# Performance work log

Hardware: AMD Instinct MI355X
Metric: run time of the kernel (lower is better)

The kernel has to match this reference:

```python
import jax, jax.numpy as jnp
import numpy as np

HIDDEN = 1280
NUM_HEADS = 16
NUM_KV_HEADS = 4
HEAD_DIM = 80
Q_SIZE = NUM_HEADS * HEAD_DIM          # 1280
KV_SIZE = NUM_KV_HEADS * HEAD_DIM      # 320
QKV_OUT = Q_SIZE + 2 * KV_SIZE         # 1920
R_SOFTPLUS_0 = 1.442695041


def setup_inputs() -> dict:
    key = jax.random.key(0)
    ks = jax.random.split(key, 6)
    B, S = 4, 2048
    return {
        "hidden_states": jax.random.normal(ks[0], (B, S, HIDDEN), dtype=jnp.float32),
        "scaling": jax.random.normal(ks[1], (HEAD_DIM,), dtype=jnp.float32),
        "qkv_w": jax.random.normal(ks[2], (QKV_OUT, HIDDEN), dtype=jnp.float32) * (1.0 / np.sqrt(HIDDEN)),
        "qkv_b": jax.random.normal(ks[3], (QKV_OUT,), dtype=jnp.float32) * 0.01,
        "o_w": jax.random.normal(ks[4], (HIDDEN, Q_SIZE), dtype=jnp.float32) * (1.0 / np.sqrt(Q_SIZE)),
        "o_b": jax.random.normal(ks[5], (HIDDEN,), dtype=jnp.float32) * 0.01,
    }


def reference(hidden_states, scaling, qkv_w, qkv_b, o_w, o_b):
    B, S, _ = hidden_states.shape
    qkv = hidden_states @ qkv_w.T + qkv_b                      # [B,S,1920]
    xq = qkv[..., :Q_SIZE].reshape(B, S, NUM_HEADS, HEAD_DIM)
    xk = qkv[..., Q_SIZE:Q_SIZE + KV_SIZE].reshape(B, S, NUM_KV_HEADS, HEAD_DIM)
    xv = qkv[..., Q_SIZE + KV_SIZE:].reshape(B, S, NUM_KV_HEADS, HEAD_DIM)
    # learned per-head-dim scaling: (r_softplus_0/sqrt(d)) * softplus(scaling)
    scale = (R_SOFTPLUS_0 / np.sqrt(HEAD_DIM)) * jax.nn.softplus(scaling)
    xq = xq * scale[None, None, None, :]
    # GQA: expand kv heads to match query heads (repeat_interleave on head dim)
    nq_per_kv = NUM_HEADS // NUM_KV_HEADS
    k = jnp.repeat(xk, nq_per_kv, axis=2)                      # [B,S,H,d]
    v = jnp.repeat(xv, nq_per_kv, axis=2)
    scores = jnp.einsum("bqhd,bkhd->bhqk", xq, k)              # [B,H,S,S]
    probs = jax.nn.softmax(scores.astype(jnp.float32), axis=-1).astype(xq.dtype)
    out = jnp.einsum("bhqk,bkhd->bqhd", probs, v)              # [B,S,H,d]
    out = out.reshape(B, S, Q_SIZE)
    return out @ o_w.T + o_b
```

## Files before the change

kernel.cpp:

```cpp
#include <hip/hip_runtime.h>

#define HIDDEN 1280
#define QOUT   1920
#define QSIZE  1280
#define KVSIZE 320
#define NHEAD  16
#define NKV    4
#define DH     80
#define SEQ    2048
#define BATCH  4
#define MTOT   (BATCH * SEQ)
#define NT64   (SEQ / 64)
#define KTILE_ELEMS 6144
#define VTILE_ELEMS 5120

typedef __attribute__((ext_vector_type(8))) short bf16x8;
typedef __attribute__((ext_vector_type(4))) short bf16x4;
typedef __attribute__((ext_vector_type(4))) float f32x4;

__device__ __forceinline__ unsigned short f2bf(float x) {
  union { float f; unsigned u; } v; v.f = x;
  unsigned r = v.u + 0x7fffu + ((v.u >> 16) & 1u);
  return (unsigned short)(r >> 16);
}

__device__ __forceinline__ unsigned packbf(float a, float b) {
  union { float f; unsigned u; } ua, ub;
  ua.f = a; ub.f = b;
  return __builtin_amdgcn_perm(ub.u + 0x8000u, ua.u + 0x8000u, 0x07060302u);
}

__device__ __forceinline__ unsigned packbf_t(float a, float b) {
  union { float f; unsigned u; } ua, ub;
  ua.f = a; ub.f = b;
  return __builtin_amdgcn_perm(ub.u, ua.u, 0x07060302u);
}

__device__ __forceinline__ float exp2x(float x) {
#if __has_builtin(__builtin_amdgcn_exp2f)
  return __builtin_amdgcn_exp2f(x);
#else
  return exp2f(x);
#endif
}

__device__ __forceinline__ void async_copy16(const void* g, void* lds) {
  __builtin_amdgcn_global_load_lds(
      (const __attribute__((address_space(1))) unsigned int*)g,
      (__attribute__((address_space(3))) unsigned int*)lds, 16, 0, 0);
}

#define HSB   (MTOT * HIDDEN / 4 / 256)
#define QWB   (QOUT * HIDDEN / 4 / 256)
#define OWB   (HIDDEN * QSIZE / 4 / 256)
__global__ __launch_bounds__(256) void prep_k(const float* __restrict__ hs,
                                              const float* __restrict__ qkv_w,
                                              const float* __restrict__ o_w,
                                              const float* __restrict__ scaling,
                                              unsigned short* __restrict__ hs_bf,
                                              unsigned short* __restrict__ qkvw_bf,
                                              unsigned short* __restrict__ ow_bf,
                                              float* __restrict__ cs) {
  const int bid = blockIdx.x, tid = threadIdx.x;
  const float* src; unsigned short* dst; int i;
  if (bid < HSB)            { src = hs;    dst = hs_bf;   i = bid * 256 + tid; }
  else if (bid < HSB + QWB) { src = qkv_w; dst = qkvw_bf; i = (bid - HSB) * 256 + tid; }
  else if (bid < HSB + QWB + OWB) { src = o_w; dst = ow_bf; i = (bid - HSB - QWB) * 256 + tid; }
  else {
    int n = (bid - HSB - QWB - OWB) * 256 + tid;
    if (n < QOUT) {
      float v = 1.0f;
      if (n < QSIZE) {
        float x = scaling[n % DH];
        float sp = (x > 20.f) ? x : log1pf(__expf(x));
        v = 1.442695041f * 1.442695041f * 0.11180339887f * sp;
      }
      cs[n] = v;
    }
    return;
  }
  float4 v = ((const float4*)src)[i];
  ushort4 o;
  o.x = f2bf(v.x); o.y = f2bf(v.y); o.z = f2bf(v.z); o.w = f2bf(v.w);
  ((ushort4*)dst)[i] = o;
}

template <int BM, bool OUT_BF16, bool USE_SCALE>
__global__ __launch_bounds__(BM * 2) void gemm_bt(const unsigned short* __restrict__ A,
                                                  const unsigned short* __restrict__ Bt,
                                                  const float* __restrict__ bias,
                                                  const float* __restrict__ colscale,
                                                  void* __restrict__ Cout,
                                                  int M, int N, int K) {
  __shared__ unsigned short As[BM * 64];
  __shared__ unsigned short Bs[128 * 64];
  const int tid  = threadIdx.x;
  const int wave = tid >> 6, lane = tid & 63;
  const int r = lane & 15, quad = lane >> 4;
  const int xm = r & 7;
  const int gx = gridDim.x;
  int lid = blockIdx.y * gx + blockIdx.x;
  const int cpx = (gx * gridDim.y) >> 3;
  lid = (lid & 7) * cpx + (lid >> 3);
  const int m0 = (lid / gx) * BM, n0 = (lid % gx) * 128;
  const int rm = (wave >> 1) * 64, cn = (wave & 1) * 64;

  f32x4 acc[4][4];
#pragma unroll
  for (int i = 0; i < 4; ++i)
#pragma unroll
    for (int j = 0; j < 4; ++j) acc[i][j] = f32x4{0.f, 0.f, 0.f, 0.f};

  for (int k0 = 0; k0 < K; k0 += 64) {
    __syncthreads();
#pragma unroll
    for (int j = 0; j < 4; ++j) {
      const int c = tid + j * (BM * 2);
      const int row = c >> 3, sp = c & 7;
      const int sd = (sp ^ (row & 7)) * 8;
      async_copy16(A + (size_t)(m0 + row) * K + k0 + sd, &As[c * 8]);
    }
#pragma unroll
    for (int j = 0; j < 512 / BM; ++j) {
      const int c = tid + j * (BM * 2);
      const int row = c >> 3, sp = c & 7;
      const int sd = (sp ^ (row & 7)) * 8;
      async_copy16(Bt + (size_t)(n0 + row) * K + k0 + sd, &Bs[c * 8]);
    }
    __syncthreads();
#pragma unroll
    for (int kk = 0; kk < 2; ++kk) {
      bf16x8 af[4], bfr[4];
#pragma unroll
      for (int mi = 0; mi < 4; ++mi)
        af[mi] = *(const bf16x8*)&As[(rm + mi * 16 + r) * 64 + ((kk * 4 + quad) ^ xm) * 8];
#pragma unroll
      for (int ni = 0; ni < 4; ++ni)
        bfr[ni] = *(const bf16x8*)&Bs[(cn + ni * 16 + r) * 64 + ((kk * 4 + quad) ^ xm) * 8];
#pragma unroll
      for (int mi = 0; mi < 4; ++mi)
#pragma unroll
        for (int ni = 0; ni < 4; ++ni)
          acc[mi][ni] = __builtin_amdgcn_mfma_f32_16x16x32_bf16(af[mi], bfr[ni], acc[mi][ni], 0, 0, 0);
    }
  }

#pragma unroll
  for (int ni = 0; ni < 4; ++ni) {
    const int n = n0 + cn + ni * 16 + r;
    const float bn = bias[n];
    const float sc = USE_SCALE ? colscale[n] : 1.0f;
#pragma unroll
    for (int mi = 0; mi < 4; ++mi) {
#pragma unroll
      for (int reg = 0; reg < 4; ++reg) {
        const int m = m0 + rm + mi * 16 + quad * 4 + reg;
        const float v = (acc[mi][ni][reg] + bn) * sc;
        if (OUT_BF16)
          ((unsigned short*)Cout)[(size_t)m * N + n] = f2bf(v);
        else
          ((float*)Cout)[(size_t)m * N + n] = v;
      }
    }
  }
}

__global__ __launch_bounds__(256) void kvpack(const unsigned short* __restrict__ qkv,
                                              unsigned short* __restrict__ Kp,
                                              unsigned short* __restrict__ Vp) {
  const int st = blockIdx.x, kvh = blockIdx.y, b = blockIdx.z;
  const int tid = threadIdx.x;
  unsigned short* kout = Kp + (size_t)((b * NKV + kvh) * NT64 + st) * KTILE_ELEMS;
#pragma unroll
  for (int j = 0; j < 3; ++j) {
    int c = tid + j * 256;
    int row = c / 12, cir = c - row * 12;
    int kk = cir >> 2, sp = cir & 3;
    int sd = sp ^ ((row >> 1) & 3);
    int d0 = kk * 32 + sd * 8;
    int skey = (row >> 5) * 32 + ((row >> 2) & 3) * 8 + ((row >> 4) & 1) * 4 + (row & 3);
    uint4 v = {0, 0, 0, 0};
    if (d0 < DH)
      v = *(const uint4*)&qkv[(size_t)(b * SEQ + st * 64 + skey) * QOUT +
                              QSIZE + kvh * DH + d0];
    *(uint4*)&kout[row * 96 + kk * 32 + sp * 8] = v;
  }
  __shared__ unsigned short tile[64][90];
  for (int c = tid; c < 640; c += 256) {
    int row = c / 10, seg = c % 10;
    uint4 v = *(const uint4*)&qkv[(size_t)(b * SEQ + st * 64 + row) * QOUT +
                                  QSIZE + KVSIZE + kvh * DH + seg * 8];
    unsigned* t32 = (unsigned*)&tile[row][seg * 8];
    t32[0] = v.x; t32[1] = v.y; t32[2] = v.z; t32[3] = v.w;
  }
  __syncthreads();
  unsigned short* vout = Vp + (size_t)((b * NKV + kvh) * NT64 + st) * VTILE_ELEMS;
  for (int c = tid; c < 5120; c += 256) {
    int d = c >> 6, key = c & 63;
    vout[d * 64 + (key ^ ((d & 7) << 3))] = tile[key][d];
  }
}

__global__ __launch_bounds__(512, 4) void attn(const unsigned short* __restrict__ qkv,
                                               const unsigned short* __restrict__ Kp,
                                               const unsigned short* __restrict__ Vp,
                                               unsigned short* __restrict__ att) {
  int qt, h, b;
  {
    int lid = (blockIdx.z * 16 + blockIdx.y) * 8 + blockIdx.x;
    lid = (lid & 7) * 64 + (lid >> 3);
    qt = lid & 7; h = (lid >> 3) & 15; b = lid >> 7;
  }
  const int kvh = h >> 2;
  const int tid = threadIdx.x;
  const int wave = tid >> 6, lane = tid & 63;
  const int r = lane & 15, quad = lane >> 4;
  const int sq8 = (quad ^ ((r >> 1) & 3)) * 8;

  __shared__ unsigned short Ks[2][64 * 96];
  __shared__ unsigned short Vs[2][80 * 64];

  const bf16x8 vone = {0x3F80, 0x3F80, 0x3F80, 0x3F80,
                       0x3F80, 0x3F80, 0x3F80, 0x3F80};

  const int qbase = qt * 256 + wave * 32;
  bf16x8 qb[2][3];
#pragma unroll
  for (int t = 0; t < 2; ++t)
#pragma unroll
    for (int kk = 0; kk < 3; ++kk)
      qb[t][kk] = *(const bf16x8*)&qkv[(size_t)(b * SEQ + qbase + t * 16 + r) * QOUT +
                                       h * DH + kk * 32 + quad * 8];

  f32x4 o_acc[6][2];
#pragma unroll
  for (int i = 0; i < 6; ++i)
#pragma unroll
    for (int t = 0; t < 2; ++t) o_acc[i][t] = f32x4{0.f, 0.f, 0.f, 0.f};

  const unsigned short* kp = Kp + (size_t)((b * NKV + kvh) * NT64) * KTILE_ELEMS;
  const unsigned short* vp = Vp + (size_t)((b * NKV + kvh) * NT64) * VTILE_ELEMS;

#define STAGE(bufi, kt_) do {                                                   \
    const unsigned short* kpt = kp + (size_t)(kt_) * KTILE_ELEMS;               \
    async_copy16(kpt + tid * 8, &Ks[bufi][tid * 8]);                            \
    if (tid < 256) async_copy16(kpt + (tid + 512) * 8, &Ks[bufi][(tid + 512) * 8]); \
    const unsigned short* vpt = vp + (size_t)(kt_) * VTILE_ELEMS;               \
    async_copy16(vpt + tid * 8, &Vs[bufi][tid * 8]);                            \
    if (tid < 128) async_copy16(vpt + (tid + 512) * 8, &Vs[bufi][(tid + 512) * 8]); \
  } while (0)

  STAGE(0, 0);
  __syncthreads();

  for (int kt = 0; kt < NT64; ++kt) {
    const int cur = kt & 1;
    if (kt + 1 < NT64) STAGE(cur ^ 1, kt + 1);

    f32x4 s[2][2][2];
    __builtin_amdgcn_s_setprio(1);
#pragma unroll
    for (int ntp = 0; ntp < 2; ++ntp)
#pragma unroll
      for (int half = 0; half < 2; ++half) {
        bf16x8 ka[3];
#pragma unroll
        for (int kk = 0; kk < 3; ++kk)
          ka[kk] = *(const bf16x8*)&Ks[cur][(ntp * 32 + half * 16 + r) * 96 + kk * 32 + sq8];
#pragma unroll
        for (int t = 0; t < 2; ++t) {
          f32x4 a0 = f32x4{0.f, 0.f, 0.f, 0.f};
#pragma unroll
          for (int kk = 0; kk < 3; ++kk)
            a0 = __builtin_amdgcn_mfma_f32_16x16x32_bf16(ka[kk], qb[t][kk], a0, 0, 0, 0);
          s[ntp][half][t] = a0;
        }
      }
    __builtin_amdgcn_s_setprio(0);

#pragma unroll
    for (int ntp = 0; ntp < 2; ++ntp) {
      uint4 pw[2];
#pragma unroll
      for (int t = 0; t < 2; ++t) {
        pw[t].x = packbf_t(exp2x(s[ntp][0][t][0]), exp2x(s[ntp][0][t][1]));
        pw[t].y = packbf_t(exp2x(s[ntp][0][t][2]), exp2x(s[ntp][0][t][3]));
        pw[t].z = packbf_t(exp2x(s[ntp][1][t][0]), exp2x(s[ntp][1][t][1]));
        pw[t].w = packbf_t(exp2x(s[ntp][1][t][2]), exp2x(s[ntp][1][t][3]));
      }
      __builtin_amdgcn_s_setprio(1);
#pragma unroll
      for (int nt2 = 0; nt2 < 5; ++nt2) {
        bf16x8 va = *(const bf16x8*)&Vs[cur][(nt2 * 16 + r) * 64 +
                                             (((ntp * 4 + quad) ^ (r & 7)) << 3)];
#pragma unroll
        for (int t = 0; t < 2; ++t) {
          union { uint4 u; bf16x8 v; } pv; pv.u = pw[t];
          o_acc[nt2][t] = __builtin_amdgcn_mfma_f32_16x16x32_bf16(va, pv.v, o_acc[nt2][t], 0, 0, 0);
        }
      }
#pragma unroll
      for (int t = 0; t < 2; ++t) {
        union { uint4 u; bf16x8 v; } pv; pv.u = pw[t];
        o_acc[5][t] = __builtin_amdgcn_mfma_f32_16x16x32_bf16(vone, pv.v, o_acc[5][t], 0, 0, 0);
      }
      __builtin_amdgcn_s_setprio(0);
    }
    __syncthreads();
  }
#undef STAGE

#pragma unroll
  for (int t = 0; t < 2; ++t) {
    const float il = 1.0f / o_acc[5][t][0];
    const size_t q = (size_t)(b * SEQ + qbase + t * 16 + r);
#pragma unroll
    for (int nt2 = 0; nt2 < 5; ++nt2) {
      uint2 w;
      w.x = packbf(o_acc[nt2][t][0] * il, o_acc[nt2][t][1] * il);
      w.y = packbf(o_acc[nt2][t][2] * il, o_acc[nt2][t][3] * il);
      *(uint2*)&att[q * QSIZE + h * DH + nt2 * 16 + quad * 4] = w;
    }
  }
}

extern "C" void kernel_launch(void* const* d_in, const int* in_sizes, int n_in,
                              void* d_out, int out_size, void* d_ws, size_t ws_size,
                              hipStream_t stream) {
  const float* hs      = (const float*)d_in[0];
  const float* scaling = (const float*)d_in[1];
  const float* qkv_w   = (const float*)d_in[2];
  const float* qkv_b   = (const float*)d_in[3];
  const float* o_w     = (const float*)d_in[4];
  const float* o_b     = (const float*)d_in[5];

  char* p = (char*)d_ws;
  unsigned short* hs_bf   = (unsigned short*)p; p += (size_t)MTOT * HIDDEN * 2;
  unsigned short* qkvw_bf = (unsigned short*)p; p += (size_t)QOUT * HIDDEN * 2;
  unsigned short* ow_bf   = (unsigned short*)p; p += (size_t)HIDDEN * QSIZE * 2;
  float* cscale           = (float*)p;          p += (size_t)QOUT * 4;
  unsigned short* qkv     = (unsigned short*)p; p += (size_t)MTOT * QOUT * 2;
  unsigned short* Kp      = (unsigned short*)p; p += (size_t)BATCH * NKV * NT64 * KTILE_ELEMS * 2;
  unsigned short* Vp      = (unsigned short*)p; p += (size_t)BATCH * NKV * NT64 * VTILE_ELEMS * 2;
  unsigned short* att     = hs_bf;

  prep_k<<<HSB + QWB + OWB + 8, 256, 0, stream>>>(hs, qkv_w, o_w, scaling,
                                                  hs_bf, qkvw_bf, ow_bf, cscale);

  dim3 g1(QOUT / 128, MTOT / 256);
  gemm_bt<256, true, true><<<g1, 512, 0, stream>>>(hs_bf, qkvw_bf, qkv_b, cscale, qkv,
                                                   MTOT, QOUT, HIDDEN);
  dim3 gp(NT64, NKV, BATCH);
  kvpack<<<gp, 256, 0, stream>>>(qkv, Kp, Vp);
  dim3 g3(SEQ / 256, NHEAD, BATCH);
  attn<<<g3, 512, 0, stream>>>(qkv, Kp, Vp, att);
  dim3 g4(QSIZE / 128, MTOT / 256);
  gemm_bt<256, false, false><<<g4, 512, 0, stream>>>(att, ow_bf, o_b, nullptr, d_out,
                                                     MTOT, QSIZE, HIDDEN);
}
```

Before: 275.8 us.

## Software-pipeline attention inner loop, interleaving exp with MFMA via sched_group_barrier

Restructures the per-tile attention loop so the exp2/pack softmax work for one 32-key half is interleaved with the QK MFMAs of the next half and the PV MFMAs of the previous half. sched_group_barrier hints (DS reads, MFMA, VALU groups) pin the instruction ordering, and the s_setprio toggles are removed. The aim is to hide transcendental VALU latency behind matrix-core work inside each wave. It raises register pressure from holding more K/V fragments live, and the fixed schedule groups may fight the compiler's own scheduling.

```diff
diff --git a/kernel.cpp b/kernel.cpp
--- a/kernel.cpp
+++ b/kernel.cpp
@@ -17,6 +17,9 @@
 typedef __attribute__((ext_vector_type(8))) short bf16x8;
 typedef __attribute__((ext_vector_type(4))) short bf16x4;
 typedef __attribute__((ext_vector_type(4))) float f32x4;
+
+#define MFMA32 __builtin_amdgcn_mfma_f32_16x16x32_bf16
+#define SGB    __builtin_amdgcn_sched_group_barrier
 
 __device__ __forceinline__ unsigned short f2bf(float x) {
   union { float f; unsigned u; } v; v.f = x;
@@ -141,7 +144,7 @@
       for (int mi = 0; mi < 4; ++mi)
 #pragma unroll
         for (int ni = 0; ni < 4; ++ni)
-          acc[mi][ni] = __builtin_amdgcn_mfma_f32_16x16x32_bf16(af[mi], bfr[ni], acc[mi][ni], 0, 0, 0);
+          acc[mi][ni] = MFMA32(af[mi], bfr[ni], acc[mi][ni], 0, 0, 0);
     }
   }
 
@@ -215,6 +218,7 @@
   const int tid = threadIdx.x;
   const int wave = tid >> 6, lane = tid & 63;
   const int r = lane & 15, quad = lane >> 4;
+  const int xm = r & 7;
   const int sq8 = (quad ^ ((r >> 1) & 3)) * 8;
 
   __shared__ unsigned short Ks[2][64 * 96];
@@ -257,55 +261,114 @@
     const int cur = kt & 1;
     if (kt + 1 < NT64) STAGE(cur ^ 1, kt + 1);
 
+    const f32x4 z = {0.f, 0.f, 0.f, 0.f};
     f32x4 s[2][2][2];
-    __builtin_amdgcn_s_setprio(1);
-#pragma unroll
-    for (int ntp = 0; ntp < 2; ++ntp)
-#pragma unroll
-      for (int half = 0; half < 2; ++half) {
-        bf16x8 ka[3];
-#pragma unroll
-        for (int kk = 0; kk < 3; ++kk)
-          ka[kk] = *(const bf16x8*)&Ks[cur][(ntp * 32 + half * 16 + r) * 96 + kk * 32 + sq8];
-#pragma unroll
-        for (int t = 0; t < 2; ++t) {
-          f32x4 a0 = f32x4{0.f, 0.f, 0.f, 0.f};
-#pragma unroll
-          for (int kk = 0; kk < 3; ++kk)
-            a0 = __builtin_amdgcn_mfma_f32_16x16x32_bf16(ka[kk], qb[t][kk], a0, 0, 0, 0);
-          s[ntp][half][t] = a0;
+
+    {
+      bf16x8 ka0[3], ka1[3];
+#pragma unroll
+      for (int kk = 0; kk < 3; ++kk) {
+        ka0[kk] = *(const bf16x8*)&Ks[cur][(0  + r) * 96 + kk * 32 + sq8];
+        ka1[kk] = *(const bf16x8*)&Ks[cur][(16 + r) * 96 + kk * 32 + sq8];
+      }
+#pragma unroll
+      for (int t = 0; t < 2; ++t) {
+        f32x4 a0 = z, a1 = z;
+#pragma unroll
+        for (int kk = 0; kk < 3; ++kk) {
+          a0 = MFMA32(ka0[kk], qb[t][kk], a0, 0, 0, 0);
+          a1 = MFMA32(ka1[kk], qb[t][kk], a1, 0, 0, 0);
         }
-      }
-    __builtin_amdgcn_s_setprio(0);
-
-#pragma unroll
-    for (int ntp = 0; ntp < 2; ++ntp) {
-      uint4 pw[2];
-#pragma unroll
-      for (int t = 0; t < 2; ++t) {
-        pw[t].x = packbf_t(exp2x(s[ntp][0][t][0]), exp2x(s[ntp][0][t][1]));
-        pw[t].y = packbf_t(exp2x(s[ntp][0][t][2]), exp2x(s[ntp][0][t][3]));
-        pw[t].z = packbf_t(exp2x(s[ntp][1][t][0]), exp2x(s[ntp][1][t][1]));
-        pw[t].w = packbf_t(exp2x(s[ntp][1][t][2]), exp2x(s[ntp][1][t][3]));
-      }
-      __builtin_amdgcn_s_setprio(1);
+        s[0][0][t] = a0; s[0][1][t] = a1;
+      }
+    }
+    SGB(0x100, 6, 0); SGB(0x008, 12, 0);
+
+    uint4 pw0[2];
+    {
+      bf16x8 kb0[3], kb1[3];
+#pragma unroll
+      for (int kk = 0; kk < 3; ++kk) {
+        kb0[kk] = *(const bf16x8*)&Ks[cur][(32 + r) * 96 + kk * 32 + sq8];
+        kb1[kk] = *(const bf16x8*)&Ks[cur][(48 + r) * 96 + kk * 32 + sq8];
+      }
+      s[1][0][0] = MFMA32(kb0[0], qb[0][0], z, 0, 0, 0);
+      pw0[0].x = packbf_t(exp2x(s[0][0][0][0]), exp2x(s[0][0][0][1]));
+      s[1][0][1] = MFMA32(kb0[0], qb[1][0], z, 0, 0, 0);
+      pw0[0].y = packbf_t(exp2x(s[0][0][0][2]), exp2x(s[0][0][0][3]));
+      s[1][1][0] = MFMA32(kb1[0], qb[0][0], z, 0, 0, 0);
+      pw0[1].x = packbf_t(exp2x(s[0][0][1][0]), exp2x(s[0][0][1][1]));
+      s[1][1][1] = MFMA32(kb1[0], qb[1][0], z, 0, 0, 0);
+      pw0[1].y = packbf_t(exp2x(s[0][0][1][2]), exp2x(s[0][0][1][3]));
+      s[1][0][0] = MFMA32(kb0[1], qb[0][1], s[1][0][0], 0, 0, 0);
+      pw0[0].z = packbf_t(exp2x(s[0][1][0][0]), exp2x(s[0][1][0][1]));
+      s[1][0][1] = MFMA32(kb0[1], qb[1][1], s[1][0][1], 0, 0, 0);
+      pw0[0].w = packbf_t(exp2x(s[0][1][0][2]), exp2x(s[0][1][0][3]));
+      s[1][1][0] = MFMA32(kb1[1], qb[0][1], s[1][1][0], 0, 0, 0);
+      pw0[1].z = packbf_t(exp2x(s[0][1][1][0]), exp2x(s[0][1][1][1]));
+      s[1][1][1] = MFMA32(kb1[1], qb[1][1], s[1][1][1], 0, 0, 0);
+      pw0[1].w = packbf_t(exp2x(s[0][1][1][2]), exp2x(s[0][1][1][3]));
+      s[1][0][0] = MFMA32(kb0[2], qb[0][2], s[1][0][0], 0, 0, 0);
+      s[1][0][1] = MFMA32(kb0[2], qb[1][2], s[1][0][1], 0, 0, 0);
+      s[1][1][0] = MFMA32(kb1[2], qb[0][2], s[1][1][0], 0, 0, 0);
+      s[1][1][1] = MFMA32(kb1[2], qb[1][2], s[1][1][1], 0, 0, 0);
+    }
+    SGB(0x100, 6, 0);
+#pragma unroll
+    for (int i = 0; i < 8; ++i) { SGB(0x008, 1, 0); SGB(0x002, 3, 0); }
+    SGB(0x008, 4, 0);
+
+    uint4 pw1[2];
+    {
+      bf16x8 va[5];
+#pragma unroll
+      for (int nt2 = 0; nt2 < 5; ++nt2)
+        va[nt2] = *(const bf16x8*)&Vs[cur][(nt2 * 16 + r) * 64 + ((quad ^ xm) << 3)];
+      union { uint4 u; bf16x8 v; } p0, p1;
+      p0.u = pw0[0]; p1.u = pw0[1];
+      o_acc[0][0] = MFMA32(va[0], p0.v, o_acc[0][0], 0, 0, 0);
+      pw1[0].x = packbf_t(exp2x(s[1][0][0][0]), exp2x(s[1][0][0][1]));
+      o_acc[0][1] = MFMA32(va[0], p1.v, o_acc[0][1], 0, 0, 0);
+      pw1[0].y = packbf_t(exp2x(s[1][0][0][2]), exp2x(s[1][0][0][3]));
+      o_acc[1][0] = MFMA32(va[1], p0.v, o_acc[1][0], 0, 0, 0);
+      pw1[1].x = packbf_t(exp2x(s[1][0][1][0]), exp2x(s[1][0][1][1]));
+      o_acc[1][1] = MFMA32(va[1], p1.v, o_acc[1][1], 0, 0, 0);
+      pw1[1].y = packbf_t(exp2x(s[1][0][1][2]), exp2x(s[1][0][1][3]));
+      o_acc[2][0] = MFMA32(va[2], p0.v, o_acc[2][0], 0, 0, 0);
+      pw1[0].z = packbf_t(exp2x(s[1][1][0][0]), exp2x(s[1][1][0][1]));
+      o_acc[2][1] = MFMA32(va[2], p1.v, o_acc[2][1], 0, 0, 0);
+      pw1[0].w = packbf_t(exp2x(s[1][1][0][2]), exp2x(s[1][1][0][3]));
+      o_acc[3][0] = MFMA32(va[3], p0.v, o_acc[3][0], 0, 0, 0);
+      pw1[1].z = packbf_t(exp2x(s[1][1][1][0]), exp2x(s[1][1][1][1]));
+      o_acc[3][1] = MFMA32(va[3], p1.v, o_acc[3][1], 0, 0, 0);
+      pw1[1].w = packbf_t(exp2x(s[1][1][1][2]), exp2x(s[1][1][1][3]));
+      o_acc[4][0] = MFMA32(va[4], p0.v, o_acc[4][0], 0, 0, 0);
+      o_acc[4][1] = MFMA32(va[4], p1.v, o_acc[4][1], 0, 0, 0);
+      o_acc[5][0] = MFMA32(vone, p0.v, o_acc[5][0], 0, 0, 0);
+      o_acc[5][1] = MFMA32(vone, p1.v, o_acc[5][1], 0, 0, 0);
+    }
+    SGB(0x100, 5, 0);
+#pragma unroll
+    for (int i = 0; i < 8; ++i) { SGB(0x008, 1, 0); SGB(0x002, 3, 0); }
+    SGB(0x008, 4, 0);
+
+    {
+      bf16x8 va[5];
+#pragma unroll
+      for (int nt2 = 0; nt2 < 5; ++nt2)
+        va[nt2] = *(const bf16x8*)&Vs[cur][(nt2 * 16 + r) * 64 + (((4 + quad) ^ xm) << 3)];
+      union { uint4 u; bf16x8 v; } p0, p1;
+      p0.u = pw1[0]; p1.u = pw1[1];
 #pragma unroll
       for (int nt2 = 0; nt2 < 5; ++nt2) {
-        bf16x8 va = *(const bf16x8*)&Vs[cur][(nt2 * 16 + r) * 64 +
-                                             (((ntp * 4 + quad) ^ (r & 7)) << 3)];
-#pragma unroll
-        for (int t = 0; t < 2; ++t) {
-          union { uint4 u; bf16x8 v; } pv; pv.u = pw[t];
-          o_acc[nt2][t] = __builtin_amdgcn_mfma_f32_16x16x32_bf16(va, pv.v, o_acc[nt2][t], 0, 0, 0);
-        }
-      }
-#pragma unroll
-      for (int t = 0; t < 2; ++t) {
-        union { uint4 u; bf16x8 v; } pv; pv.u = pw[t];
-        o_acc[5][t] = __builtin_amdgcn_mfma_f32_16x16x32_bf16(vone, pv.v, o_acc[5][t], 0, 0, 0);
-      }
-      __builtin_amdgcn_s_setprio(0);
-    }
+        o_acc[nt2][0] = MFMA32(va[nt2], p0.v, o_acc[nt2][0], 0, 0, 0);
+        o_acc[nt2][1] = MFMA32(va[nt2], p1.v, o_acc[nt2][1], 0, 0, 0);
+      }
+      o_acc[5][0] = MFMA32(vone, p0.v, o_acc[5][0], 0, 0, 0);
+      o_acc[5][1] = MFMA32(vone, p1.v, o_acc[5][1], 0, 0, 0);
+    }
+    SGB(0x100, 5, 0); SGB(0x008, 12, 0);
+
     __syncthreads();
   }
 #undef STAGE
```

Result: slower. 373.5 us (+35.5%).
